# Kernel optimization log

Hardware: AMD Instinct MI355X
Metric: run time of the kernel (lower is better)

## Reference

```python
import jax, jax.numpy as jnp
import numpy as np

B, C, LQ, D = 4096, 64, 32, 128
H = 192  # 1.5 * dim
MARGIN = 1.0
EPS = 1e-12


def l2norm(x):
    return x * jax.lax.rsqrt(jnp.maximum(jnp.sum(x * x, axis=1, keepdims=True), EPS))


def setup_inputs() -> dict:
    key = jax.random.key(0)
    ks = jax.random.split(key, 16)
    question_word_embs = jax.random.normal(ks[0], (B, LQ, D), jnp.float32)
    question_lengths = jax.random.randint(ks[1], (B,), 1, LQ + 1, jnp.int32)
    header_embs = jax.random.normal(ks[2], (B, C, D), jnp.float32)
    table_word_embs = jax.random.normal(ks[3], (B, C, D), jnp.float32)
    num_cols = jax.random.randint(ks[4], (B,), 1, C + 1, jnp.int32)
    masks = (jnp.arange(C)[None, :] < num_cols[:, None]).astype(jnp.float32)
    labels = (jax.random.uniform(ks[5], (B,)) < 0.5).astype(jnp.float32)
    # table_encoder_dense: Dense(1.5*dim, relu) -> Dense(dim, relu)
    W1 = jax.random.normal(ks[6], (2 * D, H), jnp.float32) / np.sqrt(2 * D)
    b1 = jnp.zeros((H,), jnp.float32)
    W2 = jax.random.normal(ks[7], (H, D), jnp.float32) / np.sqrt(H)
    b2 = jnp.zeros((D,), jnp.float32)
    # query LSTM(dim, activation='relu'): gate order i, f, c, o (Keras)
    Wx = jax.random.normal(ks[8], (D, 4 * D), jnp.float32) / np.sqrt(D)
    Wh = jax.random.normal(ks[9], (D, 4 * D), jnp.float32) / np.sqrt(D)
    b_lstm = jnp.zeros((4 * D,), jnp.float32)
    return dict(question_word_embs=question_word_embs, question_lengths=question_lengths,
                header_embs=header_embs, table_word_embs=table_word_embs,
                num_cols=num_cols, masks=masks, labels=labels,
                W1=W1, b1=b1, W2=W2, b2=b2, Wx=Wx, Wh=Wh, b_lstm=b_lstm)


def masked_lstm(x, lengths, Wx, Wh, b):
    # x: [B, L, D]; returns final hidden state at each row's true length
    xs = jnp.transpose(x, (1, 0, 2))  # [L, B, D]
    h0 = jnp.zeros((x.shape[0], D), x.dtype)
    c0 = jnp.zeros_like(h0)

    def step(carry, inp):
        h, c = carry
        t, x_t = inp
        z = x_t @ Wx + h @ Wh + b  # [B, 4D]
        i, f, g, o = jnp.split(z, 4, axis=1)
        i = jax.nn.sigmoid(i)
        f = jax.nn.sigmoid(f)
        g = jax.nn.relu(g)           # activation='relu'
        o = jax.nn.sigmoid(o)
        c_new = f * c + i * g
        h_new = o * jax.nn.relu(c_new)
        m = (t < lengths)[:, None].astype(x_t.dtype)
        return (m * h_new + (1 - m) * h, m * c_new + (1 - m) * c), None

    (h, _), _ = jax.lax.scan(step, (h0, c0), (jnp.arange(xs.shape[0]), xs))
    return h


def reference(question_word_embs, question_lengths, header_embs, table_word_embs,
              num_cols, masks, labels, W1, b1, W2, b2, Wx, Wh, b_lstm):
    # ---- table path ----
    flat = jnp.concatenate([header_embs.reshape(-1, D), table_word_embs.reshape(-1, D)], axis=1)  # [B*C, 2D]
    h = jax.nn.relu(flat @ W1 + b1)
    te = jax.nn.relu(h @ W2 + b2).reshape(B, C, D)
    te = te * masks[:, :, None]
    te = jnp.sum(te, axis=1) / num_cols.astype(jnp.float32)[:, None]
    te = l2norm(te)
    # ---- query path (ragged-word LSTM encoder) ----
    qe = masked_lstm(question_word_embs, question_lengths, Wx, Wh, b_lstm)
    qe = l2norm(qe)
    # ---- contrastive loss ----
    d = jnp.sum(jnp.square(qe - te), axis=1)
    d_sqrt = jnp.sqrt(d)
    loss = labels * d + (1.0 - labels) * jnp.square(jnp.maximum(0.0, MARGIN - d_sqrt))
    return 0.5 * jnp.mean(loss)
```

## Files before the change

### kernel.cpp

```cpp
#include <hip/hip_runtime.h>
#include <math.h>

#define B_  4096
#define C_  64
#define LQ_ 32
#define D_  128
#define H_  192

typedef __attribute__((ext_vector_type(8))) short bf16x8;
typedef __attribute__((ext_vector_type(4))) float f32x4;

#define KEEP(x) asm volatile("" : "+v"(x))

__device__ inline unsigned cvt_pk_bf16(float lo, float hi) {
    unsigned r;
    asm("v_cvt_pk_bf16_f32 %0, %1, %2" : "=v"(r) : "v"(lo), "v"(hi));
    return r;
}
__device__ inline short f2b(float x) { return (short)(cvt_pk_bf16(x, x) & 0xffff); }
__device__ inline float sigm(float x) { return 1.f / (1.f + __expf(-x)); }

__device__ inline void wg_barrier() {
    asm volatile("s_waitcnt lgkmcnt(0)" ::: "memory");
    __builtin_amdgcn_s_barrier();
    asm volatile("" ::: "memory");
}

__global__ __launch_bounds__(256) void prep_kernel(
    const float* __restrict__ W1, const float* __restrict__ W2,
    const float* __restrict__ Wx, const float* __restrict__ Wh,
    short* __restrict__ W1T, short* __restrict__ W2T, short* __restrict__ WTl)
{
    int idx = blockIdx.x * 256 + threadIdx.x;
    if (idx < 192 * 256) {
        int j = idx >> 8, k = idx & 255;
        W1T[idx] = f2b(W1[k * H_ + j]);
    }
    if (idx < 128 * 192) {
        int j = idx / 192, k = idx - j * 192;
        W2T[idx] = f2b(W2[k * D_ + j]);
    }
    if (idx < 512 * 256) {
        int p = idx >> 8, k = idx & 255;
        int w = p >> 6, g = (p >> 4) & 3, jj = p & 15;
        int jo = g * 128 + w * 16 + jj;
        float v = (k < 128) ? Wx[k * 512 + jo] : Wh[(k - 128) * 512 + jo];
        WTl[idx] = f2b(v);
    }
}

__global__ __launch_bounds__(512) __attribute__((amdgpu_waves_per_eu(1, 2)))
void table_kernel(
    const float* __restrict__ header, const float* __restrict__ tword,
    const float* __restrict__ masks, const int* __restrict__ num_cols,
    const short* __restrict__ W1T, const float* __restrict__ b1,
    const short* __restrict__ W2T, const float* __restrict__ b2,
    float* __restrict__ te_out)
{
    const int bb0 = blockIdx.x * 16;
    const int tid = threadIdx.x;
    const int w   = tid >> 6;
    const int l   = tid & 63;
    const int lg  = l >> 4;
    const int ln  = l & 15;
    const int ww  = w & 3;
    const int wr  = w >> 2;

    __shared__ __align__(16) short flat_s[2][32 * 256];
    __shared__ __align__(16) short h_s[32 * 192];
    __shared__ float msk_s[16][64];
    __shared__ float ncol_s[16];
    __shared__ float redv[8][128];
    __shared__ float redq[2];

    bf16x8 bw1[3][8];
    float bias1[3];
    #pragma unroll
    for (int ct = 0; ct < 3; ++ct) {
        int j = ww * 48 + ct * 16 + ln;
        bias1[ct] = b1[j];
        #pragma unroll
        for (int ks = 0; ks < 8; ++ks)
            bw1[ct][ks] = *(const bf16x8*)&W1T[j * 256 + ks * 32 + lg * 8];
    }
    bf16x8 bw2[2][6];
    float bias2[2];
    #pragma unroll
    for (int ct = 0; ct < 2; ++ct) {
        int j = ww * 32 + ct * 16 + ln;
        bias2[ct] = b2[j];
        #pragma unroll
        for (int ks = 0; ks < 6; ++ks)
            bw2[ct][ks] = *(const bf16x8*)&W2T[j * 192 + ks * 32 + lg * 8];
    }
    #pragma unroll
    for (int ct = 0; ct < 3; ++ct) {
        KEEP(bias1[ct]);
        #pragma unroll
        for (int ks = 0; ks < 8; ++ks) KEEP(bw1[ct][ks]);
    }
    #pragma unroll
    for (int ct = 0; ct < 2; ++ct) {
        KEEP(bias2[ct]);
        #pragma unroll
        for (int ks = 0; ks < 6; ++ks) KEEP(bw2[ct][ks]);
    }

    {
        int i0 = tid * 2;
        *(float2*)&((float*)msk_s)[i0] = *(const float2*)&masks[(size_t)bb0 * C_ + i0];
        if (tid < 16) ncol_s[tid] = (float)num_cols[bb0 + tid];
    }
    __syncthreads();

    float4 pf[4];
    auto issue = [&](int cc) {
        int b    = bb0 + (cc >> 1);
        int row0 = (cc & 1) * 32;
        #pragma unroll
        for (int i = 0; i < 4; ++i) {
            int idx = i * 512 + tid;
            int r   = idx >> 6;
            int c   = idx & 63;
            const float* src = (c < 32)
                ? &header[((size_t)b * C_ + row0 + r) * D_ + c * 4]
                : &tword [((size_t)b * C_ + row0 + r) * D_ + (c - 32) * 4];
            pf[i] = *(const float4*)src;
        }
    };
    issue(0);

    float csum0 = 0.f, csum1 = 0.f;

    for (int cc = 0; cc < 32; ++cc) {
        const int bi   = cc >> 1;
        const int half = cc & 1;
        char* fbuf = (char*)flat_s[cc & 1];

        #pragma unroll
        for (int i = 0; i < 4; ++i) {
            int idx = i * 512 + tid;
            int r   = idx >> 6;
            int c   = idx & 63;
            uint2 p;
            p.x = cvt_pk_bf16(pf[i].x, pf[i].y);
            p.y = cvt_pk_bf16(pf[i].z, pf[i].w);
            *(uint2*)(fbuf + r * 512 + ((c * 8) ^ ((r & 7) << 4))) = p;
        }
        if (cc + 1 < 32) issue(cc + 1);
        wg_barrier();

        {
            int row = wr * 16 + ln;
            f32x4 acc[3];
            #pragma unroll
            for (int ct = 0; ct < 3; ++ct)
                acc[ct] = (f32x4){bias1[ct], bias1[ct], bias1[ct], bias1[ct]};
            #pragma unroll
            for (int ks = 0; ks < 8; ++ks) {
                bf16x8 a = *(const bf16x8*)(fbuf + row * 512 +
                                            ((ks * 64 + lg * 16) ^ ((row & 7) << 4)));
                #pragma unroll
                for (int ct = 0; ct < 3; ++ct)
                    acc[ct] = __builtin_amdgcn_mfma_f32_16x16x32_bf16(a, bw1[ct][ks], acc[ct], 0, 0, 0);
            }
            #pragma unroll
            for (int ct = 0; ct < 3; ++ct) {
                int col = ww * 48 + ct * 16 + ln;
                #pragma unroll
                for (int reg = 0; reg < 4; ++reg) {
                    int orow = wr * 16 + lg * 4 + reg;
                    *(short*)((char*)h_s + orow * 384 + ((col * 2) ^ ((orow & 7) << 4))) =
                        f2b(fmaxf(acc[ct][reg], 0.f));
                }
            }
        }
        wg_barrier();

        {
            int row = wr * 16 + ln;
            f32x4 acc2[2];
            #pragma unroll
            for (int ct = 0; ct < 2; ++ct)
                acc2[ct] = (f32x4){bias2[ct], bias2[ct], bias2[ct], bias2[ct]};
            #pragma unroll
            for (int ks = 0; ks < 6; ++ks) {
                bf16x8 a = *(const bf16x8*)((char*)h_s + row * 384 +
                                            ((ks * 64 + lg * 16) ^ ((row & 7) << 4)));
                #pragma unroll
                for (int ct = 0; ct < 2; ++ct)
                    acc2[ct] = __builtin_amdgcn_mfma_f32_16x16x32_bf16(a, bw2[ct][ks], acc2[ct], 0, 0, 0);
            }
            #pragma unroll
            for (int reg = 0; reg < 4; ++reg) {
                int crow = half * 32 + wr * 16 + lg * 4 + reg;
                float m = msk_s[bi][crow];
                csum0 = fmaf(fmaxf(acc2[0][reg], 0.f), m, csum0);
                csum1 = fmaf(fmaxf(acc2[1][reg], 0.f), m, csum1);
            }
        }

        if (half == 1) {
            #pragma unroll
            for (int s = 16; s < 64; s <<= 1) {
                csum0 += __shfl_xor(csum0, s, 64);
                csum1 += __shfl_xor(csum1, s, 64);
            }
            if (l < 16) {
                redv[w][ww * 32 + ln]      = csum0;
                redv[w][ww * 32 + 16 + ln] = csum1;
            }
            wg_barrier();
            float v = 0.f;
            if (tid < 128) {
                int j   = tid;
                int wwj = j >> 5;
                v = (redv[wwj][j] + redv[wwj + 4][j]) / ncol_s[bi];
                float s = v * v;
                #pragma unroll
                for (int sh = 1; sh < 64; sh <<= 1) s += __shfl_xor(s, sh, 64);
                if (l == 0) redq[w] = s;
            }
            wg_barrier();
            if (tid < 128) {
                float inv = rsqrtf(fmaxf(redq[0] + redq[1], 1e-12f));
                te_out[(size_t)(bb0 + bi) * D_ + tid] = v * inv;
            }
            csum0 = 0.f; csum1 = 0.f;
        }
    }
}

__global__ __launch_bounds__(512) __attribute__((amdgpu_waves_per_eu(1, 2)))
void lstm_kernel(
    const float* __restrict__ q, const int* __restrict__ lengths,
    const short* __restrict__ WTl, const float* __restrict__ bl,
    float* __restrict__ qe_out)
{
    const int tid = threadIdx.x;
    const int b0  = blockIdx.x * 16;
    const int w   = tid >> 6;
    const int l   = tid & 63;
    const int lg  = l >> 4;
    const int ln  = l & 15;
    const int d0  = w * 16 + lg * 4;

    __shared__ __align__(16) short xh[2][16 * 256];
    __shared__ float red8[8][16];

    bf16x8 wf[4][8];
    #pragma unroll
    for (int g = 0; g < 4; ++g)
        #pragma unroll
        for (int ks = 0; ks < 8; ++ks)
            wf[g][ks] = *(const bf16x8*)&WTl[(w * 64 + g * 16 + ln) * 256 + ks * 32 + lg * 8];
    float bias[4][4];
    #pragma unroll
    for (int g = 0; g < 4; ++g)
        #pragma unroll
        for (int reg = 0; reg < 4; ++reg)
            bias[g][reg] = bl[g * 128 + d0 + reg];
    #pragma unroll
    for (int g = 0; g < 4; ++g) {
        #pragma unroll
        for (int ks = 0; ks < 8; ++ks) KEEP(wf[g][ks]);
        #pragma unroll
        for (int reg = 0; reg < 4; ++reg) KEEP(bias[g][reg]);
    }

    float creg[4] = {0.f, 0.f, 0.f, 0.f};
    float hreg[4] = {0.f, 0.f, 0.f, 0.f};
    const int len = lengths[b0 + ln];
    const int sr = tid >> 5, sc = tid & 31;

    float4 qv = *(const float4*)&q[((size_t)(b0 + sr) * LQ_ + 0) * D_ + sc * 4];

    for (int t = 0; t < LQ_; ++t) {
        char* buf = (char*)xh[t & 1];
        uint2 px; px.x = cvt_pk_bf16(qv.x, qv.y); px.y = cvt_pk_bf16(qv.z, qv.w);
        *(uint2*)(buf + sr * 512 + ((sc * 8) ^ ((sr & 7) << 4))) = px;
        uint2 ph; ph.x = cvt_pk_bf16(hreg[0], hreg[1]); ph.y = cvt_pk_bf16(hreg[2], hreg[3]);
        *(uint2*)(buf + ln * 512 + ((256 + d0 * 2) ^ ((ln & 7) << 4))) = ph;
        if (t + 1 < LQ_)
            qv = *(const float4*)&q[((size_t)(b0 + sr) * LQ_ + (t + 1)) * D_ + sc * 4];
        wg_barrier();

        f32x4 acc[4];
        #pragma unroll
        for (int g = 0; g < 4; ++g)
            acc[g] = (f32x4){bias[g][0], bias[g][1], bias[g][2], bias[g][3]};
        #pragma unroll
        for (int ks = 0; ks < 8; ++ks) {
            bf16x8 xf = *(const bf16x8*)(buf + ln * 512 + ((ks * 64 + lg * 16) ^ ((ln & 7) << 4)));
            #pragma unroll
            for (int g = 0; g < 4; ++g)
                acc[g] = __builtin_amdgcn_mfma_f32_16x16x32_bf16(wf[g][ks], xf, acc[g], 0, 0, 0);
        }

        bool live = (t < len);
        #pragma unroll
        for (int reg = 0; reg < 4; ++reg) {
            float iv = sigm(acc[0][reg]);
            float fv = sigm(acc[1][reg]);
            float gv = fmaxf(acc[2][reg], 0.f);
            float ov = sigm(acc[3][reg]);
            float cn = fmaf(fv, creg[reg], iv * gv);
            float hn = ov * fmaxf(cn, 0.f);
            if (live) { creg[reg] = cn; hreg[reg] = hn; }
        }
    }

    float sq = 0.f;
    #pragma unroll
    for (int reg = 0; reg < 4; ++reg) sq = fmaf(hreg[reg], hreg[reg], sq);
    sq += __shfl_xor(sq, 16, 64);
    sq += __shfl_xor(sq, 32, 64);
    if (l < 16) red8[w][ln] = sq;
    wg_barrier();
    float tot = 0.f;
    #pragma unroll
    for (int ww = 0; ww < 8; ++ww) tot += red8[ww][ln];
    float inv = rsqrtf(fmaxf(tot, 1e-12f));
    float4 o;
    o.x = hreg[0] * inv; o.y = hreg[1] * inv; o.z = hreg[2] * inv; o.w = hreg[3] * inv;
    *(float4*)&qe_out[(size_t)(b0 + ln) * D_ + d0] = o;
}

__global__ __launch_bounds__(64) void loss_kernel(
    const float* __restrict__ te, const float* __restrict__ qe,
    const float* __restrict__ labels, float* __restrict__ partial)
{
    const int tid = threadIdx.x;
    const int b   = blockIdx.x * 64 + tid;
    float dsum = 0.f;
    #pragma unroll 8
    for (int k4 = 0; k4 < 32; ++k4) {
        float4 a = *(const float4*)&qe[(size_t)b * D_ + k4 * 4];
        float4 c = *(const float4*)&te[(size_t)b * D_ + k4 * 4];
        float dx = a.x - c.x, dy = a.y - c.y, dz = a.z - c.z, dw = a.w - c.w;
        dsum += dx * dx + dy * dy + dz * dz + dw * dw;
    }
    float lab = labels[b];
    float ds  = sqrtf(dsum);
    float ml  = fmaxf(0.f, 1.f - ds);
    float loss = lab * dsum + (1.f - lab) * ml * ml;
    #pragma unroll
    for (int s = 32; s > 0; s >>= 1) loss += __shfl_xor(loss, s, 64);
    if (tid == 0) partial[blockIdx.x] = loss;
}

__global__ void final_kernel(const float* __restrict__ partial, float* __restrict__ out)
{
    const int tid = threadIdx.x;
    float v = partial[tid];
    #pragma unroll
    for (int s = 32; s > 0; s >>= 1) v += __shfl_xor(v, s, 64);
    if (tid == 0) out[0] = 0.5f * v / (float)B_;
}

extern "C" void kernel_launch(void* const* d_in, const int* in_sizes, int n_in,
                              void* d_out, int out_size, void* d_ws, size_t ws_size,
                              hipStream_t stream)
{
    const float* q      = (const float*)d_in[0];
    const int*   qlen   = (const int*)d_in[1];
    const float* header = (const float*)d_in[2];
    const float* tword  = (const float*)d_in[3];
    const int*   ncols  = (const int*)d_in[4];
    const float* masks  = (const float*)d_in[5];
    const float* labels = (const float*)d_in[6];
    const float* W1     = (const float*)d_in[7];
    const float* b1     = (const float*)d_in[8];
    const float* W2     = (const float*)d_in[9];
    const float* b2     = (const float*)d_in[10];
    const float* Wx     = (const float*)d_in[11];
    const float* Wh     = (const float*)d_in[12];
    const float* bl     = (const float*)d_in[13];
    float* out = (float*)d_out;

    float* te      = (float*)d_ws;
    float* qe      = te + (size_t)B_ * D_;
    float* partial = qe + (size_t)B_ * D_;
    short* W1T     = (short*)(partial + 64);
    short* W2T     = W1T + 192 * 256;
    short* WTl     = W2T + 128 * 192;

    prep_kernel<<<512, 256, 0, stream>>>(W1, W2, Wx, Wh, W1T, W2T, WTl);
    table_kernel<<<B_ / 16, 512, 0, stream>>>(header, tword, masks, ncols, W1T, b1, W2T, b2, te);
    lstm_kernel<<<B_ / 16, 512, 0, stream>>>(q, qlen, WTl, bl, qe);
    loss_kernel<<<B_ / 64, 64, 0, stream>>>(te, qe, labels, partial);
    final_kernel<<<1, 64, 0, stream>>>(partial, out);
}
```

Baseline: 136.3 us.

## Deepen global prefetch to two stages and transpose MFMA operands in table kernel

Both the table MLP kernel and the LSTM kernel now keep two register prefetch buffers and load data two iterations ahead, with the loops unrolled by two, so global load latency has more time to hide behind compute. In the table kernel the MFMA operands are swapped so each lane holds four consecutive output columns for one row. This lets the hidden activations be written to LDS as packed 8-byte stores instead of scalar shorts, and lets the column-sum reduction use in-row shuffles with a smaller shared buffer. The cost is higher register pressure from the extra prefetch buffers and per-lane bias vectors.

Result: slower. 168.5 us (+23.6%).

```diff
diff --git a/kernel.cpp b/kernel.cpp
--- a/kernel.cpp
+++ b/kernel.cpp
@@ -70,51 +70,55 @@
     __shared__ __align__(16) short h_s[32 * 192];
     __shared__ float msk_s[16][64];
     __shared__ float ncol_s[16];
-    __shared__ float redv[8][128];
+    __shared__ float redv2[2][128];
     __shared__ float redq[2];
 
     bf16x8 bw1[3][8];
-    float bias1[3];
+    float bias1[3][4];
     #pragma unroll
     for (int ct = 0; ct < 3; ++ct) {
         int j = ww * 48 + ct * 16 + ln;
-        bias1[ct] = b1[j];
         #pragma unroll
         for (int ks = 0; ks < 8; ++ks)
             bw1[ct][ks] = *(const bf16x8*)&W1T[j * 256 + ks * 32 + lg * 8];
+        #pragma unroll
+        for (int reg = 0; reg < 4; ++reg)
+            bias1[ct][reg] = b1[ww * 48 + ct * 16 + lg * 4 + reg];
     }
     bf16x8 bw2[2][6];
-    float bias2[2];
+    float bias2[2][4];
     #pragma unroll
     for (int ct = 0; ct < 2; ++ct) {
         int j = ww * 32 + ct * 16 + ln;
-        bias2[ct] = b2[j];
         #pragma unroll
         for (int ks = 0; ks < 6; ++ks)
             bw2[ct][ks] = *(const bf16x8*)&W2T[j * 192 + ks * 32 + lg * 8];
+        #pragma unroll
+        for (int reg = 0; reg < 4; ++reg)
+            bias2[ct][reg] = b2[ww * 32 + ct * 16 + lg * 4 + reg];
     }
     #pragma unroll
     for (int ct = 0; ct < 3; ++ct) {
-        KEEP(bias1[ct]);
         #pragma unroll
         for (int ks = 0; ks < 8; ++ks) KEEP(bw1[ct][ks]);
+        #pragma unroll
+        for (int reg = 0; reg < 4; ++reg) KEEP(bias1[ct][reg]);
     }
     #pragma unroll
     for (int ct = 0; ct < 2; ++ct) {
-        KEEP(bias2[ct]);
         #pragma unroll
         for (int ks = 0; ks < 6; ++ks) KEEP(bw2[ct][ks]);
-    }
-
-    {
-        int i0 = tid * 2;
-        *(float2*)&((float*)msk_s)[i0] = *(const float2*)&masks[(size_t)bb0 * C_ + i0];
-        if (tid < 16) ncol_s[tid] = (float)num_cols[bb0 + tid];
-    }
+        #pragma unroll
+        for (int reg = 0; reg < 4; ++reg) KEEP(bias2[ct][reg]);
+    }
+
+    *(float2*)&((float*)msk_s)[tid * 2] =
+        *(const float2*)&masks[(size_t)bb0 * C_ + tid * 2];
+    if (tid < 16) ncol_s[tid] = (float)num_cols[bb0 + tid];
     __syncthreads();
 
-    float4 pf[4];
-    auto issue = [&](int cc) {
+    float4 pf0[4], pf1[4];
+    auto issue = [&](int cc, float4 (&dst)[4]) {
         int b    = bb0 + (cc >> 1);
         int row0 = (cc & 1) * 32;
         #pragma unroll
@@ -125,17 +129,18 @@
             const float* src = (c < 32)
                 ? &header[((size_t)b * C_ + row0 + r) * D_ + c * 4]
                 : &tword [((size_t)b * C_ + row0 + r) * D_ + (c - 32) * 4];
-            pf[i] = *(const float4*)src;
+            dst[i] = *(const float4*)src;
         }
     };
-    issue(0);
-
-    float csum0 = 0.f, csum1 = 0.f;
-
-    for (int cc = 0; cc < 32; ++cc) {
-        const int bi   = cc >> 1;
-        const int half = cc & 1;
-        char* fbuf = (char*)flat_s[cc & 1];
+    issue(0, pf0);
+    issue(1, pf1);
+
+    float csum[2][4] = {{0.f, 0.f, 0.f, 0.f}, {0.f, 0.f, 0.f, 0.f}};
+    const int row = wr * 16 + ln;
+    const int swz = (row & 7) << 4;
+
+    auto body = [&](int cc, int half, float4 (&pfc)[4], char* fbuf) {
+        const int bi = cc >> 1;
 
         #pragma unroll
         for (int i = 0; i < 4; ++i) {
@@ -143,91 +148,96 @@
             int r   = idx >> 6;
             int c   = idx & 63;
             uint2 p;
-            p.x = cvt_pk_bf16(pf[i].x, pf[i].y);
-            p.y = cvt_pk_bf16(pf[i].z, pf[i].w);
+            p.x = cvt_pk_bf16(pfc[i].x, pfc[i].y);
+            p.y = cvt_pk_bf16(pfc[i].z, pfc[i].w);
             *(uint2*)(fbuf + r * 512 + ((c * 8) ^ ((r & 7) << 4))) = p;
         }
-        if (cc + 1 < 32) issue(cc + 1);
+        if (cc + 2 < 32) issue(cc + 2, pfc);
         wg_barrier();
 
         {
-            int row = wr * 16 + ln;
             f32x4 acc[3];
             #pragma unroll
             for (int ct = 0; ct < 3; ++ct)
-                acc[ct] = (f32x4){bias1[ct], bias1[ct], bias1[ct], bias1[ct]};
+                acc[ct] = (f32x4){bias1[ct][0], bias1[ct][1], bias1[ct][2], bias1[ct][3]};
             #pragma unroll
             for (int ks = 0; ks < 8; ++ks) {
-                bf16x8 a = *(const bf16x8*)(fbuf + row * 512 +
-                                            ((ks * 64 + lg * 16) ^ ((row & 7) << 4)));
+                bf16x8 a = *(const bf16x8*)(fbuf + row * 512 + ((ks * 64 + lg * 16) ^ swz));
                 #pragma unroll
                 for (int ct = 0; ct < 3; ++ct)
-                    acc[ct] = __builtin_amdgcn_mfma_f32_16x16x32_bf16(a, bw1[ct][ks], acc[ct], 0, 0, 0);
+                    acc[ct] = __builtin_amdgcn_mfma_f32_16x16x32_bf16(bw1[ct][ks], a, acc[ct], 0, 0, 0);
             }
             #pragma unroll
             for (int ct = 0; ct < 3; ++ct) {
-                int col = ww * 48 + ct * 16 + ln;
-                #pragma unroll
-                for (int reg = 0; reg < 4; ++reg) {
-                    int orow = wr * 16 + lg * 4 + reg;
-                    *(short*)((char*)h_s + orow * 384 + ((col * 2) ^ ((orow & 7) << 4))) =
-                        f2b(fmaxf(acc[ct][reg], 0.f));
-                }
+                int col0 = ww * 48 + ct * 16 + lg * 4;
+                uint2 hp;
+                hp.x = cvt_pk_bf16(fmaxf(acc[ct][0], 0.f), fmaxf(acc[ct][1], 0.f));
+                hp.y = cvt_pk_bf16(fmaxf(acc[ct][2], 0.f), fmaxf(acc[ct][3], 0.f));
+                *(uint2*)((char*)h_s + row * 384 + ((col0 * 2) ^ swz)) = hp;
             }
         }
         wg_barrier();
 
         {
-            int row = wr * 16 + ln;
             f32x4 acc2[2];
             #pragma unroll
             for (int ct = 0; ct < 2; ++ct)
-                acc2[ct] = (f32x4){bias2[ct], bias2[ct], bias2[ct], bias2[ct]};
+                acc2[ct] = (f32x4){bias2[ct][0], bias2[ct][1], bias2[ct][2], bias2[ct][3]};
             #pragma unroll
             for (int ks = 0; ks < 6; ++ks) {
-                bf16x8 a = *(const bf16x8*)((char*)h_s + row * 384 +
-                                            ((ks * 64 + lg * 16) ^ ((row & 7) << 4)));
+                bf16x8 a = *(const bf16x8*)((char*)h_s + row * 384 + ((ks * 64 + lg * 16) ^ swz));
                 #pragma unroll
                 for (int ct = 0; ct < 2; ++ct)
-                    acc2[ct] = __builtin_amdgcn_mfma_f32_16x16x32_bf16(a, bw2[ct][ks], acc2[ct], 0, 0, 0);
-            }
-            #pragma unroll
-            for (int reg = 0; reg < 4; ++reg) {
-                int crow = half * 32 + wr * 16 + lg * 4 + reg;
-                float m = msk_s[bi][crow];
-                csum0 = fmaf(fmaxf(acc2[0][reg], 0.f), m, csum0);
-                csum1 = fmaf(fmaxf(acc2[1][reg], 0.f), m, csum1);
-            }
+                    acc2[ct] = __builtin_amdgcn_mfma_f32_16x16x32_bf16(bw2[ct][ks], a, acc2[ct], 0, 0, 0);
+            }
+            float m = msk_s[bi][half * 32 + row];
+            #pragma unroll
+            for (int ct = 0; ct < 2; ++ct)
+                #pragma unroll
+                for (int reg = 0; reg < 4; ++reg)
+                    csum[ct][reg] = fmaf(fmaxf(acc2[ct][reg], 0.f), m, csum[ct][reg]);
         }
 
         if (half == 1) {
             #pragma unroll
-            for (int s = 16; s < 64; s <<= 1) {
-                csum0 += __shfl_xor(csum0, s, 64);
-                csum1 += __shfl_xor(csum1, s, 64);
-            }
-            if (l < 16) {
-                redv[w][ww * 32 + ln]      = csum0;
-                redv[w][ww * 32 + 16 + ln] = csum1;
+            for (int s = 1; s < 16; s <<= 1)
+                #pragma unroll
+                for (int ct = 0; ct < 2; ++ct)
+                    #pragma unroll
+                    for (int reg = 0; reg < 4; ++reg)
+                        csum[ct][reg] += __shfl_xor(csum[ct][reg], s, 64);
+            if (ln == 0) {
+                #pragma unroll
+                for (int ct = 0; ct < 2; ++ct)
+                    #pragma unroll
+                    for (int reg = 0; reg < 4; ++reg)
+                        redv2[wr][ww * 32 + ct * 16 + lg * 4 + reg] = csum[ct][reg];
             }
             wg_barrier();
             float v = 0.f;
             if (tid < 128) {
-                int j   = tid;
-                int wwj = j >> 5;
-                v = (redv[wwj][j] + redv[wwj + 4][j]) / ncol_s[bi];
-                float s = v * v;
-                #pragma unroll
-                for (int sh = 1; sh < 64; sh <<= 1) s += __shfl_xor(s, sh, 64);
-                if (l == 0) redq[w] = s;
+                v = (redv2[0][tid] + redv2[1][tid]) / ncol_s[bi];
+                float s2 = v * v;
+                #pragma unroll
+                for (int sh = 1; sh < 64; sh <<= 1) s2 += __shfl_xor(s2, sh, 64);
+                if (l == 0) redq[w] = s2;
             }
             wg_barrier();
             if (tid < 128) {
                 float inv = rsqrtf(fmaxf(redq[0] + redq[1], 1e-12f));
                 te_out[(size_t)(bb0 + bi) * D_ + tid] = v * inv;
             }
-            csum0 = 0.f; csum1 = 0.f;
-        }
+            #pragma unroll
+            for (int ct = 0; ct < 2; ++ct)
+                #pragma unroll
+                for (int reg = 0; reg < 4; ++reg)
+                    csum[ct][reg] = 0.f;
+        }
+    };
+
+    for (int bi = 0; bi < 16; ++bi) {
+        body(bi * 2,     0, pf0, (char*)flat_s[0]);
+        body(bi * 2 + 1, 1, pf1, (char*)flat_s[1]);
     }
 }
 
@@ -272,17 +282,17 @@
     float hreg[4] = {0.f, 0.f, 0.f, 0.f};
     const int len = lengths[b0 + ln];
     const int sr = tid >> 5, sc = tid & 31;
-
-    float4 qv = *(const float4*)&q[((size_t)(b0 + sr) * LQ_ + 0) * D_ + sc * 4];
-
-    for (int t = 0; t < LQ_; ++t) {
-        char* buf = (char*)xh[t & 1];
-        uint2 px; px.x = cvt_pk_bf16(qv.x, qv.y); px.y = cvt_pk_bf16(qv.z, qv.w);
+    const float* qbase = &q[((size_t)(b0 + sr) * LQ_) * D_ + sc * 4];
+
+    float4 qv0 = *(const float4*)&qbase[0 * D_];
+    float4 qv1 = *(const float4*)&qbase[1 * D_];
+
+    auto step = [&](int t, float4& qvc, char* buf) {
+        uint2 px; px.x = cvt_pk_bf16(qvc.x, qvc.y); px.y = cvt_pk_bf16(qvc.z, qvc.w);
         *(uint2*)(buf + sr * 512 + ((sc * 8) ^ ((sr & 7) << 4))) = px;
         uint2 ph; ph.x = cvt_pk_bf16(hreg[0], hreg[1]); ph.y = cvt_pk_bf16(hreg[2], hreg[3]);
         *(uint2*)(buf + ln * 512 + ((256 + d0 * 2) ^ ((ln & 7) << 4))) = ph;
-        if (t + 1 < LQ_)
-            qv = *(const float4*)&q[((size_t)(b0 + sr) * LQ_ + (t + 1)) * D_ + sc * 4];
+        if (t + 2 < LQ_) qvc = *(const float4*)&qbase[(size_t)(t + 2) * D_];
         wg_barrier();
 
         f32x4 acc[4];
@@ -308,6 +318,11 @@
             float hn = ov * fmaxf(cn, 0.f);
             if (live) { creg[reg] = cn; hreg[reg] = hn; }
         }
+    };
+
+    for (int tt = 0; tt < LQ_; tt += 2) {
+        step(tt,     qv0, (char*)xh[0]);
+        step(tt + 1, qv1, (char*)xh[1]);
     }
 
     float sq = 0.f;
```
